# Optimization experiments

Hardware: AMD Instinct MI355X
Metric: run time of the kernel (lower is better)

## Reference

```python
import jax, jax.numpy as jnp
import numpy as np

HEADS, DH = 8, 32

def _ln(x):
    m = x.mean(-1, keepdims=True)
    v = ((x - m) ** 2).mean(-1, keepdims=True)
    return (x - m) * jax.lax.rsqrt(v + 1e-5)

def _attn(xq, xk, ei, ea, wq, wk, wv, we, wo):
    # one relation: q from dst-type nodes xq, k/v from src-type nodes xk
    Nd, Ns, E = xq.shape[0], xk.shape[0], ea.shape[0]
    src, dst = ei[0], ei[1]
    q = (xq @ wq).reshape(Nd, HEADS, DH)
    k = (xk @ wk).reshape(Ns, HEADS, DH)
    v = (xk @ wv).reshape(Ns, HEADS, DH)
    e = (ea @ we).reshape(E, HEADS, DH)
    s = jnp.sum(q[dst] * (k[src] + e), axis=-1) * (DH ** -0.5)  # (E, heads)
    m = jax.ops.segment_max(s, dst, num_segments=Nd)
    m = jnp.where(jnp.isfinite(m), m, 0.0)
    ex = jnp.exp(s - m[dst])
    den = jax.ops.segment_sum(ex, dst, num_segments=Nd)
    msg = jax.ops.segment_sum(ex[:, :, None] * (v[src] + e), dst, num_segments=Nd)
    msg = msg / (den[:, :, None] + 1e-9)
    return msg.reshape(Nd, HEADS * DH) @ wo

def setup_inputs() -> dict:
    key = jax.random.key(0)
    ks = list(jax.random.split(key, 24))
    N, H, ED, L, F = 18432, 256, 64, 2, 512
    EA, ES = 294912, 65536
    nrm = lambda k, shp, s=1.0: jax.random.normal(k, shp, dtype=jnp.float32) * s
    inp = {}
    inp['all_feats_left'] = nrm(ks[0], (N, H))
    inp['all_feats_right'] = nrm(ks[1], (N, H))
    inp['ea_ll'] = nrm(ks[2], (EA, ED))
    inp['ea_rr'] = nrm(ks[3], (EA, ED))
    inp['ea_lr'] = nrm(ks[4], (ES, ED))
    inp['ea_rl'] = nrm(ks[5], (ES, ED))
    inp['ei_ll'] = jax.random.randint(ks[6], (2, EA), 0, N, dtype=jnp.int32)
    inp['ei_rr'] = jax.random.randint(ks[7], (2, EA), 0, N, dtype=jnp.int32)
    inp['ei_lr'] = jax.random.randint(ks[8], (2, ES), 0, N, dtype=jnp.int32)
    inp['ei_rl'] = jax.random.randint(ks[9], (2, ES), 0, N, dtype=jnp.int32)
    # relation order: 0=ll, 1=rr, 2=lr (src left -> dst right), 3=rl
    inp['Wq'] = nrm(ks[10], (L, 4, H, H), H ** -0.5)
    inp['Wk'] = nrm(ks[11], (L, 4, H, H), H ** -0.5)
    inp['Wv'] = nrm(ks[12], (L, 4, H, H), H ** -0.5)
    inp['We'] = nrm(ks[13], (L, 4, ED, H), ED ** -0.5)
    inp['Wo'] = nrm(ks[14], (L, 4, H, H), H ** -0.5)
    inp['ffn_w1'] = nrm(ks[15], (L, 2, H, F), H ** -0.5)
    inp['ffn_b1'] = jnp.zeros((L, 2, F), jnp.float32)
    inp['ffn_w2'] = nrm(ks[16], (L, 2, F, H), F ** -0.5)
    inp['ffn_b2'] = jnp.zeros((L, 2, H), jnp.float32)
    inp['head_w1'] = nrm(ks[17], (H, H), H ** -0.5)
    inp['head_b1'] = jnp.zeros((H,), jnp.float32)
    inp['head_w2'] = nrm(ks[18], (H, 7), H ** -0.5)
    inp['head_b2'] = jnp.zeros((7,), jnp.float32)
    inp['action_start'] = 2048  # slice(K, None), K current nodes per arm
    return inp

def reference(all_feats_left, all_feats_right, ea_ll, ea_rr, ea_lr, ea_rl,
              Wq, Wk, Wv, We, Wo, ffn_w1, ffn_b1, ffn_w2, ffn_b2,
              head_w1, head_b1, head_w2, head_b2,
              ei_ll, ei_rr, ei_lr, ei_rl, action_start):
    xl, xr = all_feats_left, all_feats_right
    L = Wq.shape[0]
    for l in range(L):
        agg_l = (_attn(xl, xl, ei_ll, ea_ll, Wq[l, 0], Wk[l, 0], Wv[l, 0], We[l, 0], Wo[l, 0])
                 + _attn(xl, xr, ei_rl, ea_rl, Wq[l, 3], Wk[l, 3], Wv[l, 3], We[l, 3], Wo[l, 3]))
        agg_r = (_attn(xr, xr, ei_rr, ea_rr, Wq[l, 1], Wk[l, 1], Wv[l, 1], We[l, 1], Wo[l, 1])
                 + _attn(xr, xl, ei_lr, ea_lr, Wq[l, 2], Wk[l, 2], Wv[l, 2], We[l, 2], Wo[l, 2]))
        xl = _ln(xl + agg_l)
        xr = _ln(xr + agg_r)
        xl = _ln(xl + jax.nn.gelu(xl @ ffn_w1[l, 0] + ffn_b1[l, 0]) @ ffn_w2[l, 0] + ffn_b2[l, 0])
        xr = _ln(xr + jax.nn.gelu(xr @ ffn_w1[l, 1] + ffn_b1[l, 1]) @ ffn_w2[l, 1] + ffn_b2[l, 1])
    la = xl[action_start:]
    ra = xr[action_start:]
    head = lambda z: jax.nn.gelu(z @ head_w1 + head_b1) @ head_w2 + head_b2
    return head(la), head(ra)
```

## Files before the change

### kernel.cpp

```cpp
#include <hip/hip_runtime.h>
#include <math.h>

typedef __attribute__((ext_vector_type(8))) short short8;
typedef __attribute__((ext_vector_type(4))) float f32x4;

__device__ __forceinline__ unsigned short f2bf(float f) {
  unsigned u = __builtin_bit_cast(unsigned, f);
  u += 0x7fff + ((u >> 16) & 1);
  return (unsigned short)(u >> 16);
}
__device__ __forceinline__ float bf2f(unsigned short h) {
  unsigned u = ((unsigned)h) << 16;
  return __builtin_bit_cast(float, u);
}
__device__ __forceinline__ float gelu_f(float x) {
  const float c0 = 0.7978845608028654f;
  return 0.5f * x * (1.0f + tanhf(c0 * (x + 0.044715f * x * x * x)));
}
__device__ __forceinline__ void gload16(const unsigned short* g, unsigned short* l) {
  __builtin_amdgcn_global_load_lds(
      (const __attribute__((address_space(1))) unsigned int*)g,
      (__attribute__((address_space(3))) unsigned int*)l, 16, 0, 0);
}
__device__ __forceinline__ int ileave512(int cc) {
  const int base = (cc & 256) ? 4 : 0;
  const int c2 = cc & 255;
  return (c2 >> 2) * 8 + base + (c2 & 3);
}

__device__ __forceinline__ void kloop_db(
    const unsigned short* gA0, const unsigned short* gA1,
    const unsigned short* gB0, const unsigned short* gB1,
    unsigned short* As, unsigned short* Bs,
    int lo0, int lo1, const int* roffA, const int* roffB,
    f32x4 (&acc)[4][4], int K)
{
  gload16(gA0, As + lo0);
  gload16(gA1, As + lo1);
  gload16(gB0, Bs + lo0);
  gload16(gB1, Bs + lo1);
  int cur = 0;
  for (int k0 = 32; k0 < K; k0 += 32) {
    const int nb = (cur ^ 1) * 4096;
    gload16(gA0 + k0, As + nb + lo0);
    gload16(gA1 + k0, As + nb + lo1);
    gload16(gB0 + k0, Bs + nb + lo0);
    gload16(gB1 + k0, Bs + nb + lo1);
    __builtin_amdgcn_sched_barrier(0);
    asm volatile("s_waitcnt vmcnt(4)" ::: "memory");
    __builtin_amdgcn_s_barrier();
    __builtin_amdgcn_sched_barrier(0);
    const int cb = cur * 4096;
    short8 af[4], bfr[4];
#pragma unroll
    for (int m = 0; m < 4; ++m) af[m] = *(const short8*)(As + cb + roffA[m]);
#pragma unroll
    for (int n = 0; n < 4; ++n) bfr[n] = *(const short8*)(Bs + cb + roffB[n]);
#pragma unroll
    for (int m = 0; m < 4; ++m)
#pragma unroll
      for (int n = 0; n < 4; ++n)
        acc[m][n] = __builtin_amdgcn_mfma_f32_16x16x32_bf16(af[m], bfr[n], acc[m][n], 0, 0, 0);
    __builtin_amdgcn_sched_barrier(0);
    __builtin_amdgcn_s_barrier();
    cur ^= 1;
  }
  __builtin_amdgcn_sched_barrier(0);
  asm volatile("s_waitcnt vmcnt(0)" ::: "memory");
  __builtin_amdgcn_s_barrier();
  __builtin_amdgcn_sched_barrier(0);
  const int cb = cur * 4096;
  short8 af[4], bfr[4];
#pragma unroll
  for (int m = 0; m < 4; ++m) af[m] = *(const short8*)(As + cb + roffA[m]);
#pragma unroll
  for (int n = 0; n < 4; ++n) bfr[n] = *(const short8*)(Bs + cb + roffB[n]);
#pragma unroll
  for (int m = 0; m < 4; ++m)
#pragma unroll
    for (int n = 0; n < 4; ++n)
      acc[m][n] = __builtin_amdgcn_mfma_f32_16x16x32_bf16(af[m], bfr[n], acc[m][n], 0, 0, 0);
}

__global__ __launch_bounds__(256)
void gemm_qkv_k(const unsigned short* __restrict__ A0, const unsigned short* __restrict__ A1,
                const unsigned short* __restrict__ BT0, const unsigned short* __restrict__ BT1,
                unsigned short* __restrict__ qT0, unsigned short* __restrict__ qT1,
                unsigned short* __restrict__ kvS0, unsigned short* __restrict__ kvS1,
                unsigned short* __restrict__ kvX0, unsigned short* __restrict__ kvX1,
                int M)
{
  const int z = blockIdx.z;
  const unsigned short* A  = z ? A1  : A0;
  const unsigned short* BT = z ? BT1 : BT0;
  unsigned short* qT  = z ? qT1  : qT0;
  unsigned short* kvS = z ? kvS1 : kvS0;
  unsigned short* kvX = z ? kvX1 : kvX0;
  const int K = 256, lda = 256;

  __shared__ __align__(16) unsigned short As[2 * 4096];
  __shared__ __align__(16) unsigned short Bs[2 * 4096];
  const int tid = threadIdx.x;
  const int bm = blockIdx.x * 128, bn = blockIdx.y * 128;
  const int lane = tid & 63, w = tid >> 6;
  const int wr = w >> 1, wc = w & 1;
  const int l15 = lane & 15, kg = lane >> 4;
  const int srow0 = w * 16 + (lane >> 2);
  const int srow1 = 64 + srow0;
  const int sslot = lane & 3;
  const int koff0 = (((sslot - (srow0 >> 1)) & 3)) * 8;
  const int koff1 = (((sslot - (srow1 >> 1)) & 3)) * 8;
  const unsigned short* gA0 = A + (size_t)(bm + srow0) * lda + koff0;
  const unsigned short* gA1 = A + (size_t)(bm + srow1) * lda + koff1;
  const unsigned short* gB0 = BT + (size_t)(bn + srow0) * K + koff0;
  const unsigned short* gB1 = BT + (size_t)(bn + srow1) * K + koff1;
  const int lo0 = w * 512;
  const int lo1 = 2048 + w * 512;

  int roffA[4], roffB[4];
#pragma unroll
  for (int m = 0; m < 4; ++m) {
    int row = wr * 64 + m * 16 + l15;
    roffA[m] = row * 32 + ((kg + (row >> 1)) & 3) * 8;
  }
#pragma unroll
  for (int n = 0; n < 4; ++n) {
    int col = wc * 64 + n * 16 + l15;
    roffB[n] = col * 32 + ((kg + (col >> 1)) & 3) * 8;
  }

  f32x4 acc[4][4] = {};
  kloop_db(gA0, gA1, gB0, gB1, As, Bs, lo0, lo1, roffA, roffB, acc, K);

#pragma unroll
  for (int m = 0; m < 4; ++m) {
#pragma unroll
    for (int n = 0; n < 4; ++n) {
      int col = bn + wc * 64 + n * 16 + l15;
      f32x4 v = acc[m][n];
#pragma unroll
      for (int r2 = 0; r2 < 4; ++r2) {
        int row = bm + wr * 64 + m * 16 + kg * 4 + r2;
        unsigned short bv = f2bf(v[r2]);
        if (col < 768) {
          qT[(size_t)row * 1536 + col] = bv;
        } else if (col < 1280) {
          kvS[(size_t)row * 512 + ileave512(col - 768)] = bv;
        } else if (col < 2048) {
          qT[(size_t)row * 1536 + 768 + (col - 1280)] = bv;
        } else {
          kvX[(size_t)row * 512 + ileave512(col - 2048)] = bv;
        }
      }
    }
  }
}

template<bool BIAS, bool GELU>
__global__ __launch_bounds__(256)
void gemm_mfma2_k(const unsigned short* __restrict__ A0, const unsigned short* __restrict__ A1,
                  int lda,
                  const unsigned short* __restrict__ BT0, const unsigned short* __restrict__ BT1,
                  const float* __restrict__ bias0, const float* __restrict__ bias1,
                  float* __restrict__ Cf0, float* __restrict__ Cf1, int Sf, int ldf,
                  unsigned short* __restrict__ Cb10, unsigned short* __restrict__ Cb11,
                  int S2, int ldb1,
                  unsigned short* __restrict__ Cb20, unsigned short* __restrict__ Cb21, int ldb2,
                  int M, int N, int K)
{
  const int z = blockIdx.z;
  const unsigned short* A  = z ? A1  : A0;
  const unsigned short* BT = z ? BT1 : BT0;
  const float* bias        = z ? bias1 : bias0;
  float* Cf                = z ? Cf1 : Cf0;
  unsigned short* Cb1      = z ? Cb11 : Cb10;
  unsigned short* Cb2      = z ? Cb21 : Cb20;

  __shared__ __align__(16) unsigned short As[2 * 4096];
  __shared__ __align__(16) unsigned short Bs[2 * 4096];
  const int tid = threadIdx.x;
  const int bm = blockIdx.x * 128, bn = blockIdx.y * 128;
  const int lane = tid & 63, w = tid >> 6;
  const int wr = w >> 1, wc = w & 1;
  const int l15 = lane & 15, kg = lane >> 4;
  const int srow0 = w * 16 + (lane >> 2);
  const int srow1 = 64 + srow0;
  const int sslot = lane & 3;
  const int koff0 = (((sslot - (srow0 >> 1)) & 3)) * 8;
  const int koff1 = (((sslot - (srow1 >> 1)) & 3)) * 8;
  const unsigned short* gA0 = A + (size_t)(bm + srow0) * lda + koff0;
  const unsigned short* gA1 = A + (size_t)(bm + srow1) * lda + koff1;
  const unsigned short* gB0 = BT + (size_t)(bn + srow0) * K + koff0;
  const unsigned short* gB1 = BT + (size_t)(bn + srow1) * K + koff1;
  const int lo0 = w * 512;
  const int lo1 = 2048 + w * 512;

  int roffA[4], roffB[4];
#pragma unroll
  for (int m = 0; m < 4; ++m) {
    int row = wr * 64 + m * 16 + l15;
    roffA[m] = row * 32 + ((kg + (row >> 1)) & 3) * 8;
  }
#pragma unroll
  for (int n = 0; n < 4; ++n) {
    int col = wc * 64 + n * 16 + l15;
    roffB[n] = col * 32 + ((kg + (col >> 1)) & 3) * 8;
  }

  f32x4 acc[4][4] = {};
  kloop_db(gA0, gA1, gB0, gB1, As, Bs, lo0, lo1, roffA, roffB, acc, K);

#pragma unroll
  for (int m = 0; m < 4; ++m) {
#pragma unroll
    for (int n = 0; n < 4; ++n) {
      int col = bn + wc * 64 + n * 16 + l15;
      float bv = BIAS ? bias[col] : 0.f;
      f32x4 v = acc[m][n];
#pragma unroll
      for (int r2 = 0; r2 < 4; ++r2) {
        int row = bm + wr * 64 + m * 16 + kg * 4 + r2;
        float val = v[r2] + bv;
        if (GELU) val = gelu_f(val);
        if (col < Sf) {
          Cf[(size_t)row * ldf + col] = val;
        } else if (col < S2) {
          Cb1[(size_t)row * ldb1 + (col - Sf)] = f2bf(val);
        } else {
          Cb2[(size_t)row * ldb2 + (col - S2)] = f2bf(val);
        }
      }
    }
  }
}

template<bool BIAS>
__global__ __launch_bounds__(256)
void gemm_k2(const float* __restrict__ A0, const float* __restrict__ A1,
             const float* __restrict__ B, const float* __restrict__ bias,
             float* __restrict__ C0, float* __restrict__ C1,
             int M, int N, int K)
{
  const float* A = blockIdx.z ? A1 : A0;
  float* C = blockIdx.z ? C1 : C0;
  __shared__ float As[16][132];
  __shared__ float Bs[16][132];
  const int tid = threadIdx.x;
  const int tx = tid & 15, ty = tid >> 4;
  const int bm = blockIdx.x * 128;
  float acc[8][8];
#pragma unroll
  for (int i = 0; i < 8; ++i)
#pragma unroll
    for (int j = 0; j < 8; ++j) acc[i][j] = 0.f;
  const int ar = tid >> 1;
  const int ac = (tid & 1) * 8;
  const int br = tid >> 4;
  const int bc = (tid & 15) * 8;
  for (int k0 = 0; k0 < K; k0 += 16) {
    {
      float av[8] = {0,0,0,0,0,0,0,0};
      if (bm + ar < M) {
        const float* app = A + (size_t)(bm + ar) * K + (k0 + ac);
        float4 a0 = *(const float4*)app;
        float4 a1 = *(const float4*)(app + 4);
        av[0]=a0.x; av[1]=a0.y; av[2]=a0.z; av[3]=a0.w;
        av[4]=a1.x; av[5]=a1.y; av[6]=a1.z; av[7]=a1.w;
      }
#pragma unroll
      for (int i = 0; i < 8; ++i) As[ac + i][ar] = av[i];
    }
    {
      float bv[8] = {0,0,0,0,0,0,0,0};
      const float* bpp = B + (size_t)(k0 + br) * N + bc;
#pragma unroll
      for (int i = 0; i < 8; ++i) { if (bc + i < N) bv[i] = bpp[i]; }
#pragma unroll
      for (int i = 0; i < 8; ++i) Bs[br][bc + i] = bv[i];
    }
    __syncthreads();
#pragma unroll
    for (int kk = 0; kk < 16; ++kk) {
      float a[8], b[8];
      float4 t0 = *(const float4*)&As[kk][ty * 8];
      float4 t1 = *(const float4*)&As[kk][ty * 8 + 4];
      float4 u0 = *(const float4*)&Bs[kk][tx * 8];
      float4 u1 = *(const float4*)&Bs[kk][tx * 8 + 4];
      a[0]=t0.x;a[1]=t0.y;a[2]=t0.z;a[3]=t0.w;a[4]=t1.x;a[5]=t1.y;a[6]=t1.z;a[7]=t1.w;
      b[0]=u0.x;b[1]=u0.y;b[2]=u0.z;b[3]=u0.w;b[4]=u1.x;b[5]=u1.y;b[6]=u1.z;b[7]=u1.w;
#pragma unroll
      for (int i = 0; i < 8; ++i)
#pragma unroll
        for (int j = 0; j < 8; ++j)
          acc[i][j] = fmaf(a[i], b[j], acc[i][j]);
    }
    __syncthreads();
  }
#pragma unroll
  for (int i = 0; i < 8; ++i) {
    int row = bm + ty * 8 + i;
    if (row >= M) continue;
    int colg = tx * 8;
    float* cp = C + (size_t)row * N + colg;
#pragma unroll
    for (int j = 0; j < 8; ++j) {
      int cc = colg + j;
      if (cc < N) {
        float val = acc[i][j];
        if (BIAS) val += bias[cc];
        cp[j] = val;
      }
    }
  }
}

__global__ void tc_k(const float* __restrict__ in, unsigned short* __restrict__ out,
                     int K, int N, int inStride, int outStride, int rowOff, int totK, int kOff)
{
  const int mat = blockIdx.y;
  const int idx = blockIdx.x * 256 + threadIdx.x;
  if (idx >= N * K) return;
  const int n = idx / K, k = idx - n * K;
  out[(size_t)mat * outStride + (size_t)(rowOff + n) * totK + kOff + k] =
      f2bf(in[(size_t)mat * inStride + (size_t)k * N + n]);
}

__global__ void tc_all_k(const float* __restrict__ Wq, const float* __restrict__ Wk,
                         const float* __restrict__ Wv, unsigned short* __restrict__ BTall)
{
  const int part = blockIdx.z;
  const int slot = blockIdx.y;
  const int l = slot >> 1, zz = slot & 1;
  const int self = l * 4 + zz;
  const int crossq = l * 4 + (zz ? 2 : 3);
  const int crosskv = l * 4 + (zz ? 3 : 2);
  const float* in; int mat, rowOff;
  switch (part) {
    case 0: in = Wq; mat = self;    rowOff = 0;    break;
    case 1: in = Wk; mat = self;    rowOff = 768;  break;
    case 2: in = Wv; mat = self;    rowOff = 1024; break;
    case 3: in = Wq; mat = crossq;  rowOff = 1280; break;
    case 4: in = Wk; mat = crosskv; rowOff = 2048; break;
    default:in = Wv; mat = crosskv; rowOff = 2304; break;
  }
  const int idx = blockIdx.x * 256 + threadIdx.x;
  const int n = idx >> 8, k = idx & 255;
  BTall[(size_t)slot * 655360 + (size_t)(rowOff + n) * 256 + k] =
      f2bf(in[(size_t)mat * 65536 + (size_t)k * 256 + n]);
}

__global__ __launch_bounds__(256)
void wqe2_k(unsigned short* __restrict__ BTall, const float* __restrict__ We)
{
  const int which = blockIdx.z;
  const int slot = blockIdx.y;
  const int l = slot >> 1, zz = slot & 1;
  const int mat = which ? (l * 4 + (zz ? 2 : 3)) : (l * 4 + zz);
  const int baseQ = which ? 1280 : 0;
  const int baseT = which ? 1536 : 256;
  const int oc = blockIdx.x;
  const int g = oc >> 6, cc = oc & 63;
  const int kin = threadIdx.x;
  const float* wrow = We + (size_t)mat * 16384 + (size_t)cc * 256 + g * 32;
  const unsigned short* bq = BTall + (size_t)slot * 655360 + (size_t)(baseQ + g * 32) * 256 + kin;
  float acc = 0.f;
#pragma unroll 8
  for (int d = 0; d < 32; ++d)
    acc += bf2f(bq[(size_t)d * 256]) * wrow[d];
  BTall[(size_t)slot * 655360 + (size_t)(baseT + oc) * 256 + kin] = f2bf(acc);
}

__global__ void wo_tc_k(const float* __restrict__ Wo, unsigned short* __restrict__ BTwoF)
{
  const int mat = blockIdx.y;
  const int idx = blockIdx.x * 256 + threadIdx.x;
  const int n = idx >> 8, k = idx & 255;
  const int l = mat >> 2, i = mat & 3;
  const int side = (i == 1 || i == 2) ? 1 : 0;
  const int base = (i >= 2) ? 768 : 0;
  BTwoF[(size_t)(l * 2 + side) * 393216 + (size_t)n * 1536 + base + k] =
      f2bf(Wo[(size_t)mat * 65536 + (size_t)k * 256 + n]);
}

__global__ __launch_bounds__(256)
void wc_k(const float* __restrict__ We, const float* __restrict__ Wo,
          unsigned short* __restrict__ BTwoF)
{
  const int mat = blockIdx.y;
  const int j = blockIdx.x;
  const int h = j >> 6, c = j & 63;
  const int n = threadIdx.x;
  const float* wep = We + (size_t)mat * 16384 + (size_t)c * 256 + h * 32;
  const float* wop = Wo + (size_t)mat * 65536 + (size_t)(h * 32) * 256 + n;
  float acc = 0.f;
#pragma unroll 8
  for (int d = 0; d < 32; ++d)
    acc += wep[d] * wop[(size_t)d * 256];
  const int l = mat >> 2, i = mat & 3;
  const int side = (i == 1 || i == 2) ? 1 : 0;
  const int base = (i >= 2) ? 768 : 0;
  BTwoF[(size_t)(l * 2 + side) * 393216 + (size_t)n * 1536 + base + 256 + j] = f2bf(acc);
}

__global__ __launch_bounds__(256)
void edge4_k(const int* __restrict__ o0, const int* __restrict__ o1,
             const int* __restrict__ o2, const int* __restrict__ o3,
             const int2* __restrict__ p0, const int2* __restrict__ p1,
             const int2* __restrict__ p2, const int2* __restrict__ p3,
             const float* __restrict__ e0, const float* __restrict__ e1,
             const float* __restrict__ e2, const float* __restrict__ e3,
             unsigned short* q0, unsigned short* q1,
             unsigned short* q2, unsigned short* q3,
             const unsigned short* __restrict__ k0, const unsigned short* __restrict__ k1,
             const unsigned short* __restrict__ k2, const unsigned short* __restrict__ k3,
             int Nn)
{
  const int y = blockIdx.y;
  const int* offs = (y == 0) ? o0 : (y == 1) ? o1 : (y == 2) ? o2 : o3;
  const int2* pairs = (y == 0) ? p0 : (y == 1) ? p1 : (y == 2) ? p2 : p3;
  const float* ea = (y == 0) ? e0 : (y == 1) ? e1 : (y == 2) ? e2 : e3;
  unsigned short* qTmsg = (y == 0) ? q0 : (y == 1) ? q1 : (y == 2) ? q2 : q3;
  const unsigned short* kv = (y == 0) ? k0 : (y == 1) ? k1 : (y == 2) ? k2 : k3;
  const int wv = (blockIdx.x * blockDim.x + threadIdx.x) >> 6;
  if (wv >= Nn) return;
  const int lane = threadIdx.x & 63;
  const int g = lane >> 3, p = lane & 7;
  const float scale = 0.17677669529663687f;
  const ushort4 qu = *(const ushort4*)(qTmsg + (size_t)wv * 1536 + lane * 4);
  const float qx = bf2f(qu.x), qy = bf2f(qu.y), qz = bf2f(qu.z), qw = bf2f(qu.w);
  const unsigned short* Tp = qTmsg + (size_t)wv * 1536 + 256 + g * 64 + p * 8;
  const ushort4 tu0 = *(const ushort4*)Tp;
  const ushort4 tu1 = *(const ushort4*)(Tp + 4);
  const float Ta0 = bf2f(tu0.x), Ta1 = bf2f(tu0.y), Ta2 = bf2f(tu0.z), Ta3 = bf2f(tu0.w);
  const float Tc0 = bf2f(tu1.x), Tc1 = bf2f(tu1.y), Tc2 = bf2f(tu1.z), Tc3 = bf2f(tu1.w);
  float m = -INFINITY, den = 0.f;
  float ax = 0.f, ay = 0.f, az = 0.f, aw = 0.f;
  float G[8] = {0,0,0,0,0,0,0,0};
  const int e0i = __builtin_amdgcn_readfirstlane(offs[wv]);
  const int e1i = __builtin_amdgcn_readfirstlane(offs[wv + 1]);
  for (int j = e0i; j < e1i; j += 2) {
    const bool hasB = (j + 1) < e1i;
    const int2 prA = pairs[j];
    const int2 prB = hasB ? pairs[j + 1] : prA;
    const f32x4* epA = (const f32x4*)(ea + (size_t)prA.x * 64 + p * 8);
    const f32x4* epB = (const f32x4*)(ea + (size_t)prB.x * 64 + p * 8);
    const f32x4 a0 = __builtin_nontemporal_load(epA);
    const f32x4 a1 = __builtin_nontemporal_load(epA + 1);
    const f32x4 b0 = __builtin_nontemporal_load(epB);
    const f32x4 b1 = __builtin_nontemporal_load(epB + 1);
    const short8 kvA = *(const short8*)(kv + (size_t)prA.y * 512 + lane * 8);
    const short8 kvB = *(const short8*)(kv + (size_t)prB.y * 512 + lane * 8);
    float pA = qx * bf2f((unsigned short)kvA[0]) + qy * bf2f((unsigned short)kvA[1])
             + qz * bf2f((unsigned short)kvA[2]) + qw * bf2f((unsigned short)kvA[3]);
    pA += a0[0]*Ta0 + a0[1]*Ta1 + a0[2]*Ta2 + a0[3]*Ta3;
    pA += a1[0]*Tc0 + a1[1]*Tc1 + a1[2]*Tc2 + a1[3]*Tc3;
    float pB = qx * bf2f((unsigned short)kvB[0]) + qy * bf2f((unsigned short)kvB[1])
             + qz * bf2f((unsigned short)kvB[2]) + qw * bf2f((unsigned short)kvB[3]);
    pB += b0[0]*Ta0 + b0[1]*Ta1 + b0[2]*Ta2 + b0[3]*Ta3;
    pB += b1[0]*Tc0 + b1[1]*Tc1 + b1[2]*Tc2 + b1[3]*Tc3;
    pA += __shfl_xor(pA, 1, 64); pA += __shfl_xor(pA, 2, 64); pA += __shfl_xor(pA, 4, 64);
    pB += __shfl_xor(pB, 1, 64); pB += __shfl_xor(pB, 2, 64); pB += __shfl_xor(pB, 4, 64);
    const float sA = pA * scale;
    const float sB = hasB ? pB * scale : -INFINITY;
    const float mn = fmaxf(m, fmaxf(sA, sB));
    const float corr = __expf(m - mn);
    const float wA = __expf(sA - mn);
    const float wB = __expf(sB - mn);
    m = mn;
    den = den * corr + wA + wB;
    ax = ax * corr + wA * bf2f((unsigned short)kvA[4]) + wB * bf2f((unsigned short)kvB[4]);
    ay = ay * corr + wA * bf2f((unsigned short)kvA[5]) + wB * bf2f((unsigned short)kvB[5]);
    az = az * corr + wA * bf2f((unsigned short)kvA[6]) + wB * bf2f((unsigned short)kvB[6]);
    aw = aw * corr + wA * bf2f((unsigned short)kvA[7]) + wB * bf2f((unsigned short)kvB[7]);
    G[0] = G[0] * corr + wA * a0[0] + wB * b0[0];
    G[1] = G[1] * corr + wA * a0[1] + wB * b0[1];
    G[2] = G[2] * corr + wA * a0[2] + wB * b0[2];
    G[3] = G[3] * corr + wA * a0[3] + wB * b0[3];
    G[4] = G[4] * corr + wA * a1[0] + wB * b1[0];
    G[5] = G[5] * corr + wA * a1[1] + wB * b1[1];
    G[6] = G[6] * corr + wA * a1[2] + wB * b1[2];
    G[7] = G[7] * corr + wA * a1[3] + wB * b1[3];
  }
  const float inv = 1.f / (den + 1e-9f);
  ushort4 o;
  o.x = f2bf(ax * inv); o.y = f2bf(ay * inv);
  o.z = f2bf(az * inv); o.w = f2bf(aw * inv);
  *(ushort4*)(qTmsg + (size_t)wv * 1536 + lane * 4) = o;
  short8 gn;
#pragma unroll
  for (int i = 0; i < 8; ++i) gn[i] = (short)f2bf(G[i] * inv);
  *(short8*)(qTmsg + (size_t)wv * 1536 + 256 + g * 64 + p * 8) = gn;
}

__global__ __launch_bounds__(256)
void add_ln2_k(unsigned short* __restrict__ xbL, const unsigned short* __restrict__ addL,
               unsigned short* __restrict__ xbR, const unsigned short* __restrict__ addR, int Nn)
{
  unsigned short* xb = blockIdx.y ? xbR : xbL;
  const unsigned short* add = blockIdx.y ? addR : addL;
  const int wv = (blockIdx.x * blockDim.x + threadIdx.x) >> 6;
  if (wv >= Nn) return;
  const int lane = threadIdx.x & 63;
  ushort4 xu = *(const ushort4*)(xb + (size_t)wv * 256 + lane * 4);
  ushort4 au = *(const ushort4*)(add + (size_t)wv * 256 + lane * 4);
  float4 y;
  y.x = bf2f(xu.x) + bf2f(au.x); y.y = bf2f(xu.y) + bf2f(au.y);
  y.z = bf2f(xu.z) + bf2f(au.z); y.w = bf2f(xu.w) + bf2f(au.w);
  float s = y.x + y.y + y.z + y.w;
#pragma unroll
  for (int msk = 1; msk < 64; msk <<= 1) s += __shfl_xor(s, msk, 64);
  const float mean = s * (1.f / 256.f);
  float4 d;
  d.x = y.x - mean; d.y = y.y - mean; d.z = y.z - mean; d.w = y.w - mean;
  float sq = d.x*d.x + d.y*d.y + d.z*d.z + d.w*d.w;
#pragma unroll
  for (int msk = 1; msk < 64; msk <<= 1) sq += __shfl_xor(sq, msk, 64);
  const float r = rsqrtf(sq * (1.f / 256.f) + 1e-5f);
  ushort4 ob;
  ob.x = f2bf(d.x * r); ob.y = f2bf(d.y * r);
  ob.z = f2bf(d.z * r); ob.w = f2bf(d.w * r);
  *(ushort4*)(xb + (size_t)wv * 256 + lane * 4) = ob;
}

__global__ void cvt_x2_k(const float* __restrict__ aL, unsigned short* __restrict__ xbL,
                         const float* __restrict__ aR, unsigned short* __restrict__ xbR, int n4)
{
  const float* a = blockIdx.y ? aR : aL;
  unsigned short* xb = blockIdx.y ? xbR : xbL;
  int i = blockIdx.x * 256 + threadIdx.x;
  if (i >= n4) return;
  float4 v = ((const float4*)a)[i];
  ushort4 b;
  b.x = f2bf(v.x); b.y = f2bf(v.y); b.z = f2bf(v.z); b.w = f2bf(v.w);
  ((ushort4*)xb)[i] = b;
}

__global__ void zero4_k(int* p, int n) {
  int i = blockIdx.x * 256 + threadIdx.x;
  if (i < n) p[i] = 0;
}
__global__ void hist4_k(const int* d0, const int* d1, const int* d2, const int* d3,
                        int E0, int E1, int E2, int E3, int* cnt, int Nn) {
  const int s = blockIdx.y;
  const int* d = (s == 0) ? d0 : (s == 1) ? d1 : (s == 2) ? d2 : d3;
  const int E = (s == 0) ? E0 : (s == 1) ? E1 : (s == 2) ? E2 : E3;
  int e = blockIdx.x * 256 + threadIdx.x;
  if (e < E) atomicAdd(&cnt[s * Nn + d[e]], 1);
}
__global__ __launch_bounds__(256)
void scan4_k(const int* __restrict__ cnt, int* __restrict__ offs, int* __restrict__ cursor, int Nn)
{
  __shared__ int sums[256];
  const int s = blockIdx.x;
  const int t = threadIdx.x;
  const int* c = cnt + (size_t)s * Nn;
  int* o = offs + (size_t)s * (Nn + 1);
  int* cur = cursor + (size_t)s * Nn;
  const int chunk = (Nn + 255) / 256;
  const int base = t * chunk;
  int sl = 0;
  for (int i = 0; i < chunk; ++i) {
    int idx = base + i;
    if (idx < Nn) sl += c[idx];
  }
  sums[t] = sl;
  __syncthreads();
  for (int off = 1; off < 256; off <<= 1) {
    int val = (t >= off) ? sums[t - off] : 0;
    __syncthreads();
    sums[t] += val;
    __syncthreads();
  }
  int run = (t == 0) ? 0 : sums[t - 1];
  for (int i = 0; i < chunk; ++i) {
    int idx = base + i;
    if (idx < Nn) { o[idx] = run; cur[idx] = run; run += c[idx]; }
  }
  if (t == 255) o[Nn] = run;
}
__global__ void scatter4_k(const int* e0p, const int* e1p, const int* e2p, const int* e3p,
                           int E0, int E1, int E2, int E3, int* cursor,
                           int2* p0, int2* p1, int2* p2, int2* p3, int Nn) {
  const int s = blockIdx.y;
  const int* ei = (s == 0) ? e0p : (s == 1) ? e1p : (s == 2) ? e2p : e3p;
  int2* po = (s == 0) ? p0 : (s == 1) ? p1 : (s == 2) ? p2 : p3;
  const int E = (s == 0) ? E0 : (s == 1) ? E1 : (s == 2) ? E2 : E3;
  int e = blockIdx.x * 256 + threadIdx.x;
  if (e < E) {
    int pos = atomicAdd(&cursor[s * Nn + ei[E + e]], 1);
    po[pos] = make_int2(e, ei[e]);
  }
}

extern "C" void kernel_launch(void* const* d_in, const int* in_sizes, int n_in,
                              void* d_out, int out_size, void* d_ws, size_t ws_size,
                              hipStream_t stream)
{
  (void)n_in; (void)ws_size;
  const float* afl = (const float*)d_in[0];
  const float* afr = (const float*)d_in[1];
  const float* eaA[4] = {(const float*)d_in[2], (const float*)d_in[3],
                         (const float*)d_in[4], (const float*)d_in[5]};
  const int* eiA[4] = {(const int*)d_in[6], (const int*)d_in[7],
                       (const int*)d_in[8], (const int*)d_in[9]};
  const float* Wq  = (const float*)d_in[10];
  const float* Wk  = (const float*)d_in[11];
  const float* Wv  = (const float*)d_in[12];
  const float* We  = (const float*)d_in[13];
  const float* Wo  = (const float*)d_in[14];
  const float* fw1 = (const float*)d_in[15];
  const float* fb1 = (const float*)d_in[16];
  const float* fw2 = (const float*)d_in[17];
  const float* fb2 = (const float*)d_in[18];
  const float* hw1 = (const float*)d_in[19];
  const float* hb1 = (const float*)d_in[20];
  const float* hw2 = (const float*)d_in[21];
  const float* hb2 = (const float*)d_in[22];

  const int Nn = in_sizes[0] / 256;
  const int E[4] = {in_sizes[2] / 64, in_sizes[3] / 64, in_sizes[4] / 64, in_sizes[5] / 64};
  const int Mh = out_size / 14;
  const int astart = Nn - Mh;
  float* out = (float*)d_out;

  char* wsp = (char*)d_ws;
  auto alloc = [&](size_t bytes) -> void* {
    void* pp = (void*)wsp;
    wsp += (bytes + 255) & ~(size_t)255;
    return pp;
  };
  unsigned short* xlb = (unsigned short*)alloc((size_t)Nn * 256 * 2);
  unsigned short* xrb = (unsigned short*)alloc((size_t)Nn * 256 * 2);
  unsigned short* aggLb = (unsigned short*)alloc((size_t)Nn * 256 * 2);
  unsigned short* aggRb = (unsigned short*)alloc((size_t)Nn * 256 * 2);
  unsigned short* qTmsgA = (unsigned short*)alloc((size_t)Nn * 1536 * 2);
  unsigned short* qTmsgB = (unsigned short*)alloc((size_t)Nn * 1536 * 2);
  unsigned short* kvSA = (unsigned short*)alloc((size_t)Nn * 512 * 2);
  unsigned short* kvSB = (unsigned short*)alloc((size_t)Nn * 512 * 2);
  unsigned short* kvXL = (unsigned short*)alloc((size_t)Nn * 512 * 2);
  unsigned short* kvXR = (unsigned short*)alloc((size_t)Nn * 512 * 2);
  unsigned short* BTall = (unsigned short*)alloc((size_t)4 * 655360 * 2);
  unsigned short* BTwoF = (unsigned short*)alloc((size_t)4 * 256 * 1536 * 2);
  unsigned short* BTf1  = (unsigned short*)alloc((size_t)4 * 512 * 256 * 2);
  unsigned short* BTf2  = (unsigned short*)alloc((size_t)4 * 256 * 512 * 2);
  unsigned short* BTh1  = (unsigned short*)alloc((size_t)256 * 256 * 2);
  int* offs4 = (int*)alloc((size_t)4 * (Nn + 1) * 4);
  int* cnt4  = (int*)alloc((size_t)4 * Nn * 4);
  int* cur4  = (int*)alloc((size_t)4 * Nn * 4);
  int2* pairs[4];
  for (int s = 0; s < 4; ++s) pairs[s] = (int2*)alloc((size_t)E[s] * 8);

  const dim3 B256(256);
  const int wgNodes = (Nn * 64 + 255) / 256;
  int maxE = E[0];
  for (int s = 1; s < 4; ++s) if (E[s] > maxE) maxE = E[s];

  cvt_x2_k<<<dim3((Nn * 64 + 255) / 256, 2), B256, 0, stream>>>(afl, xlb, afr, xrb, Nn * 64);
  zero4_k<<<dim3((4 * Nn + 255) / 256), B256, 0, stream>>>(cnt4, 4 * Nn);
  {
    dim3 gh((maxE + 255) / 256, 4);
    hist4_k<<<gh, B256, 0, stream>>>(eiA[0] + E[0], eiA[1] + E[1], eiA[2] + E[2], eiA[3] + E[3],
                                     E[0], E[1], E[2], E[3], cnt4, Nn);
    scan4_k<<<dim3(4), B256, 0, stream>>>(cnt4, offs4, cur4, Nn);
    scatter4_k<<<gh, B256, 0, stream>>>(eiA[0], eiA[1], eiA[2], eiA[3],
                                        E[0], E[1], E[2], E[3], cur4,
                                        pairs[0], pairs[1], pairs[2], pairs[3], Nn);
  }
  {
    tc_all_k<<<dim3(256, 4, 6), B256, 0, stream>>>(Wq, Wk, Wv, BTall);
    wqe2_k<<<dim3(512, 4, 2), B256, 0, stream>>>(BTall, We);
    wo_tc_k<<<dim3(256, 8), B256, 0, stream>>>(Wo, BTwoF);
    wc_k<<<dim3(512, 8), B256, 0, stream>>>(We, Wo, BTwoF);
    tc_k<<<dim3((131072 + 255) / 256, 4), B256, 0, stream>>>(fw1, BTf1, 256, 512, 131072, 131072, 0, 256, 0);
    tc_k<<<dim3((131072 + 255) / 256, 4), B256, 0, stream>>>(fw2, BTf2, 512, 256, 131072, 131072, 0, 512, 0);
    tc_k<<<dim3((65536 + 255) / 256, 1), B256, 0, stream>>>(hw1, BTh1, 256, 256, 0, 0, 0, 256, 0);
  }

  auto mfma2 = [&](const unsigned short* A0, const unsigned short* A1, int lda,
                   const unsigned short* BT0, const unsigned short* BT1,
                   const float* bias0, const float* bias1,
                   float* Cf0, float* Cf1, int Sf, int ldf,
                   unsigned short* Cb10, unsigned short* Cb11, int S2, int ldb1,
                   unsigned short* Cb20, unsigned short* Cb21, int ldb2,
                   int M, int N, int K, bool biasf, bool gelu) {
    dim3 g(M / 128, N / 128, 2);
    if (biasf && gelu)
      gemm_mfma2_k<true, true ><<<g, B256, 0, stream>>>(A0, A1, lda, BT0, BT1, bias0, bias1,
          Cf0, Cf1, Sf, ldf, Cb10, Cb11, S2, ldb1, Cb20, Cb21, ldb2, M, N, K);
    else if (biasf)
      gemm_mfma2_k<true, false><<<g, B256, 0, stream>>>(A0, A1, lda, BT0, BT1, bias0, bias1,
          Cf0, Cf1, Sf, ldf, Cb10, Cb11, S2, ldb1, Cb20, Cb21, ldb2, M, N, K);
    else
      gemm_mfma2_k<false, false><<<g, B256, 0, stream>>>(A0, A1, lda, BT0, BT1, bias0, bias1,
          Cf0, Cf1, Sf, ldf, Cb10, Cb11, S2, ldb1, Cb20, Cb21, ldb2, M, N, K);
  };

  for (int l = 0; l < 2; ++l) {
    gemm_qkv_k<<<dim3(Nn / 128, 20, 2), B256, 0, stream>>>(
        xlb, xrb,
        BTall + (size_t)(l * 2 + 0) * 655360, BTall + (size_t)(l * 2 + 1) * 655360,
        qTmsgA, qTmsgB, kvSA, kvSB, kvXL, kvXR, Nn);
    edge4_k<<<dim3(wgNodes, 4), B256, 0, stream>>>(
        offs4, offs4 + (size_t)(Nn + 1), offs4 + (size_t)3 * (Nn + 1), offs4 + (size_t)2 * (Nn + 1),
        pairs[0], pairs[1], pairs[3], pairs[2],
        eaA[0], eaA[1], eaA[3], eaA[2],
        qTmsgA, qTmsgB, qTmsgA + 768, qTmsgB + 768,
        kvSA, kvSB, kvXR, kvXL, Nn);
    mfma2(qTmsgA, qTmsgB, 1536, BTwoF + (size_t)(l*2+0)*393216, BTwoF + (size_t)(l*2+1)*393216,
          nullptr, nullptr, nullptr, nullptr, 0, 0, aggLb, aggRb, 256, 256,
          nullptr, nullptr, 0, Nn, 256, 1536, false, false);
    add_ln2_k<<<dim3(wgNodes, 2), B256, 0, stream>>>(xlb, aggLb, xrb, aggRb, Nn);
    const int fL = l * 2 + 0, fR = l * 2 + 1;
    mfma2(xlb, xrb, 256, BTf1 + (size_t)fL*131072, BTf1 + (size_t)fR*131072,
          fb1 + (size_t)fL*512, fb1 + (size_t)fR*512, nullptr, nullptr, 0, 0,
          kvSA, kvSB, 512, 512, nullptr, nullptr, 0, Nn, 512, 256, true, true);
    mfma2(kvSA, kvSB, 512, BTf2 + (size_t)fL*131072, BTf2 + (size_t)fR*131072,
          fb2 + (size_t)fL*256, fb2 + (size_t)fR*256, nullptr, nullptr, 0, 0,
          aggLb, aggRb, 256, 256, nullptr, nullptr, 0, Nn, 256, 512, true, false);
    add_ln2_k<<<dim3(wgNodes, 2), B256, 0, stream>>>(xlb, aggLb, xrb, aggRb, Nn);
  }
  float* h1L = (float*)kvSA;
  float* h1R = (float*)kvSB;
  mfma2(xlb + (size_t)astart * 256, xrb + (size_t)astart * 256, 256, BTh1, BTh1,
        hb1, hb1, h1L, h1R, 256, 256, nullptr, nullptr, 0, 0, nullptr, nullptr, 0,
        Mh, 256, 256, true, true);
  gemm_k2<true><<<dim3(Mh / 128, 1, 2), B256, 0, stream>>>(h1L, h1R, hw2, hb2,
                                                           out, out + (size_t)Mh * 7, Mh, 7, 256);
}
```

Baseline: 1.029 ms.

## Fuse output-projection and FFN2 GEMMs with residual add and LayerNorm

Adds a GEMM kernel whose block covers 64 full rows of 256 columns, so the epilogue can add the residual, reduce the row mean and variance across waves through shared memory, and write the normalized bf16 result in place. It replaces the separate Wo GEMM, FFN2 GEMM and add_ln2 kernels, removing the bf16 agg intermediate round trips and two launches per layer. The cost is a narrower grid (Nn/64 blocks per arm) with a single wave column per block, one-pass variance (E[x²]−mean²), and residual loads that are not coalesced.

```diff
diff --git a/kernel.cpp b/kernel.cpp
--- a/kernel.cpp
+++ b/kernel.cpp
@@ -80,6 +80,149 @@
 #pragma unroll
     for (int n = 0; n < 4; ++n)
       acc[m][n] = __builtin_amdgcn_mfma_f32_16x16x32_bf16(af[m], bfr[n], acc[m][n], 0, 0, 0);
+}
+
+template<bool BIAS>
+__global__ __launch_bounds__(256)
+void gemm_ln_k(const unsigned short* __restrict__ A0, const unsigned short* __restrict__ A1,
+               int lda,
+               const unsigned short* __restrict__ BT0, const unsigned short* __restrict__ BT1,
+               const float* __restrict__ bias0, const float* __restrict__ bias1,
+               unsigned short* __restrict__ xb0, unsigned short* __restrict__ xb1,
+               int K)
+{
+  const int z = blockIdx.z;
+  const unsigned short* A  = z ? A1 : A0;
+  const unsigned short* BT = z ? BT1 : BT0;
+  const float* bias        = z ? bias1 : bias0;
+  unsigned short* xb       = z ? xb1 : xb0;
+
+  __shared__ __align__(16) unsigned short As[2 * 2048];
+  __shared__ __align__(16) unsigned short Bs[2 * 8192];
+  __shared__ float redS[64][4];
+  __shared__ float redQ[64][4];
+
+  const int tid = threadIdx.x;
+  const int bm = blockIdx.x * 64;
+  const int lane = tid & 63, w = tid >> 6;
+  const int l15 = lane & 15, kg = lane >> 4;
+  const int sslot = lane & 3;
+  const int srowA = w * 16 + (lane >> 2);
+  const int koffA = ((sslot - (srowA >> 1)) & 3) * 8;
+  const unsigned short* gA = A + (size_t)(bm + srowA) * lda + koffA;
+  const int loA = w * 512;
+  const unsigned short* gB[4];
+  int loB[4];
+#pragma unroll
+  for (int h = 0; h < 4; ++h) {
+    int srowB = h * 64 + w * 16 + (lane >> 2);
+    int koffB = ((sslot - (srowB >> 1)) & 3) * 8;
+    gB[h] = BT + (size_t)srowB * K + koffB;
+    loB[h] = h * 2048 + w * 512;
+  }
+  int roffA[4], roffB[4];
+#pragma unroll
+  for (int m = 0; m < 4; ++m) {
+    int row = m * 16 + l15;
+    roffA[m] = row * 32 + ((kg + (row >> 1)) & 3) * 8;
+  }
+#pragma unroll
+  for (int n = 0; n < 4; ++n) {
+    int col = w * 64 + n * 16 + l15;
+    roffB[n] = col * 32 + ((kg + (col >> 1)) & 3) * 8;
+  }
+
+  f32x4 acc[4][4] = {};
+  gload16(gA, As + loA);
+#pragma unroll
+  for (int h = 0; h < 4; ++h) gload16(gB[h], Bs + loB[h]);
+  int cur = 0;
+  for (int k0 = 32; k0 < K; k0 += 32) {
+    const int nbA = (cur ^ 1) * 2048, nbB = (cur ^ 1) * 8192;
+    gload16(gA + k0, As + nbA + loA);
+#pragma unroll
+    for (int h = 0; h < 4; ++h) gload16(gB[h] + k0, Bs + nbB + loB[h]);
+    __builtin_amdgcn_sched_barrier(0);
+    asm volatile("s_waitcnt vmcnt(5)" ::: "memory");
+    __builtin_amdgcn_s_barrier();
+    __builtin_amdgcn_sched_barrier(0);
+    const int cbA = cur * 2048, cbB = cur * 8192;
+    short8 af[4], bfr[4];
+#pragma unroll
+    for (int m = 0; m < 4; ++m) af[m] = *(const short8*)(As + cbA + roffA[m]);
+#pragma unroll
+    for (int n = 0; n < 4; ++n) bfr[n] = *(const short8*)(Bs + cbB + roffB[n]);
+#pragma unroll
+    for (int m = 0; m < 4; ++m)
+#pragma unroll
+      for (int n = 0; n < 4; ++n)
+        acc[m][n] = __builtin_amdgcn_mfma_f32_16x16x32_bf16(af[m], bfr[n], acc[m][n], 0, 0, 0);
+    __builtin_amdgcn_sched_barrier(0);
+    __builtin_amdgcn_s_barrier();
+    cur ^= 1;
+  }
+  __builtin_amdgcn_sched_barrier(0);
+  asm volatile("s_waitcnt vmcnt(0)" ::: "memory");
+  __builtin_amdgcn_s_barrier();
+  __builtin_amdgcn_sched_barrier(0);
+  {
+    const int cbA = cur * 2048, cbB = cur * 8192;
+    short8 af[4], bfr[4];
+#pragma unroll
+    for (int m = 0; m < 4; ++m) af[m] = *(const short8*)(As + cbA + roffA[m]);
+#pragma unroll
+    for (int n = 0; n < 4; ++n) bfr[n] = *(const short8*)(Bs + cbB + roffB[n]);
+#pragma unroll
+    for (int m = 0; m < 4; ++m)
+#pragma unroll
+      for (int n = 0; n < 4; ++n)
+        acc[m][n] = __builtin_amdgcn_mfma_f32_16x16x32_bf16(af[m], bfr[n], acc[m][n], 0, 0, 0);
+  }
+
+  float bv[4];
+#pragma unroll
+  for (int n = 0; n < 4; ++n) bv[n] = BIAS ? bias[w * 64 + n * 16 + l15] : 0.f;
+
+#pragma unroll
+  for (int m = 0; m < 4; ++m) {
+#pragma unroll
+    for (int r2 = 0; r2 < 4; ++r2) {
+      const int row = m * 16 + kg * 4 + r2;
+      float rs = 0.f, rq = 0.f;
+#pragma unroll
+      for (int n = 0; n < 4; ++n) {
+        const int col = w * 64 + n * 16 + l15;
+        float val = acc[m][n][r2] + bv[n]
+                  + bf2f(xb[(size_t)(bm + row) * 256 + col]);
+        acc[m][n][r2] = val;
+        rs += val;
+        rq += val * val;
+      }
+      rs += __shfl_xor(rs, 1, 64); rq += __shfl_xor(rq, 1, 64);
+      rs += __shfl_xor(rs, 2, 64); rq += __shfl_xor(rq, 2, 64);
+      rs += __shfl_xor(rs, 4, 64); rq += __shfl_xor(rq, 4, 64);
+      rs += __shfl_xor(rs, 8, 64); rq += __shfl_xor(rq, 8, 64);
+      if (l15 == 0) { redS[row][w] = rs; redQ[row][w] = rq; }
+    }
+  }
+  __syncthreads();
+#pragma unroll
+  for (int m = 0; m < 4; ++m) {
+#pragma unroll
+    for (int r2 = 0; r2 < 4; ++r2) {
+      const int row = m * 16 + kg * 4 + r2;
+      const float s = redS[row][0] + redS[row][1] + redS[row][2] + redS[row][3];
+      const float q = redQ[row][0] + redQ[row][1] + redQ[row][2] + redQ[row][3];
+      const float mean = s * (1.f / 256.f);
+      const float var = q * (1.f / 256.f) - mean * mean;
+      const float r = rsqrtf(var + 1e-5f);
+#pragma unroll
+      for (int n = 0; n < 4; ++n) {
+        const int col = w * 64 + n * 16 + l15;
+        xb[(size_t)(bm + row) * 256 + col] = f2bf((acc[m][n][r2] - mean) * r);
+      }
+    }
+  }
 }
 
 __global__ __launch_bounds__(256)
@@ -215,12 +358,12 @@
 #pragma unroll
     for (int n = 0; n < 4; ++n) {
       int col = bn + wc * 64 + n * 16 + l15;
-      float bv = BIAS ? bias[col] : 0.f;
+      float bvv = BIAS ? bias[col] : 0.f;
       f32x4 v = acc[m][n];
 #pragma unroll
       for (int r2 = 0; r2 < 4; ++r2) {
         int row = bm + wr * 64 + m * 16 + kg * 4 + r2;
-        float val = v[r2] + bv;
+        float val = v[r2] + bvv;
         if (GELU) val = gelu_f(val);
         if (col < Sf) {
           Cf[(size_t)row * ldf + col] = val;
@@ -271,12 +414,12 @@
       for (int i = 0; i < 8; ++i) As[ac + i][ar] = av[i];
     }
     {
-      float bv[8] = {0,0,0,0,0,0,0,0};
+      float bvv[8] = {0,0,0,0,0,0,0,0};
       const float* bpp = B + (size_t)(k0 + br) * N + bc;
 #pragma unroll
-      for (int i = 0; i < 8; ++i) { if (bc + i < N) bv[i] = bpp[i]; }
-#pragma unroll
-      for (int i = 0; i < 8; ++i) Bs[br][bc + i] = bv[i];
+      for (int i = 0; i < 8; ++i) { if (bc + i < N) bvv[i] = bpp[i]; }
+#pragma unroll
+      for (int i = 0; i < 8; ++i) Bs[br][bc + i] = bvv[i];
     }
     __syncthreads();
 #pragma unroll
@@ -492,36 +635,6 @@
   *(short8*)(qTmsg + (size_t)wv * 1536 + 256 + g * 64 + p * 8) = gn;
 }
 
-__global__ __launch_bounds__(256)
-void add_ln2_k(unsigned short* __restrict__ xbL, const unsigned short* __restrict__ addL,
-               unsigned short* __restrict__ xbR, const unsigned short* __restrict__ addR, int Nn)
-{
-  unsigned short* xb = blockIdx.y ? xbR : xbL;
-  const unsigned short* add = blockIdx.y ? addR : addL;
-  const int wv = (blockIdx.x * blockDim.x + threadIdx.x) >> 6;
-  if (wv >= Nn) return;
-  const int lane = threadIdx.x & 63;
-  ushort4 xu = *(const ushort4*)(xb + (size_t)wv * 256 + lane * 4);
-  ushort4 au = *(const ushort4*)(add + (size_t)wv * 256 + lane * 4);
-  float4 y;
-  y.x = bf2f(xu.x) + bf2f(au.x); y.y = bf2f(xu.y) + bf2f(au.y);
-  y.z = bf2f(xu.z) + bf2f(au.z); y.w = bf2f(xu.w) + bf2f(au.w);
-  float s = y.x + y.y + y.z + y.w;
-#pragma unroll
-  for (int msk = 1; msk < 64; msk <<= 1) s += __shfl_xor(s, msk, 64);
-  const float mean = s * (1.f / 256.f);
-  float4 d;
-  d.x = y.x - mean; d.y = y.y - mean; d.z = y.z - mean; d.w = y.w - mean;
-  float sq = d.x*d.x + d.y*d.y + d.z*d.z + d.w*d.w;
-#pragma unroll
-  for (int msk = 1; msk < 64; msk <<= 1) sq += __shfl_xor(sq, msk, 64);
-  const float r = rsqrtf(sq * (1.f / 256.f) + 1e-5f);
-  ushort4 ob;
-  ob.x = f2bf(d.x * r); ob.y = f2bf(d.y * r);
-  ob.z = f2bf(d.z * r); ob.w = f2bf(d.w * r);
-  *(ushort4*)(xb + (size_t)wv * 256 + lane * 4) = ob;
-}
-
 __global__ void cvt_x2_k(const float* __restrict__ aL, unsigned short* __restrict__ xbL,
                          const float* __restrict__ aR, unsigned short* __restrict__ xbR, int n4)
 {
@@ -631,8 +744,6 @@
   };
   unsigned short* xlb = (unsigned short*)alloc((size_t)Nn * 256 * 2);
   unsigned short* xrb = (unsigned short*)alloc((size_t)Nn * 256 * 2);
-  unsigned short* aggLb = (unsigned short*)alloc((size_t)Nn * 256 * 2);
-  unsigned short* aggRb = (unsigned short*)alloc((size_t)Nn * 256 * 2);
   unsigned short* qTmsgA = (unsigned short*)alloc((size_t)Nn * 1536 * 2);
   unsigned short* qTmsgB = (unsigned short*)alloc((size_t)Nn * 1536 * 2);
   unsigned short* kvSA = (unsigned short*)alloc((size_t)Nn * 512 * 2);
@@ -644,6 +755,8 @@
   unsigned short* BTf1  = (unsigned short*)alloc((size_t)4 * 512 * 256 * 2);
   unsigned short* BTf2  = (unsigned short*)alloc((size_t)4 * 256 * 512 * 2);
   unsigned short* BTh1  = (unsigned short*)alloc((size_t)256 * 256 * 2);
+  float* h1L = (float*)alloc((size_t)Mh * 256 * 4);
+  float* h1R = (float*)alloc((size_t)Mh * 256 * 4);
   int* offs4 = (int*)alloc((size_t)4 * (Nn + 1) * 4);
   int* cnt4  = (int*)alloc((size_t)4 * Nn * 4);
   int* cur4  = (int*)alloc((size_t)4 * Nn * 4);
@@ -706,21 +819,19 @@
         eaA[0], eaA[1], eaA[3], eaA[2],
         qTmsgA, qTmsgB, qTmsgA + 768, qTmsgB + 768,
         kvSA, kvSB, kvXR, kvXL, Nn);
-    mfma2(qTmsgA, qTmsgB, 1536, BTwoF + (size_t)(l*2+0)*393216, BTwoF + (size_t)(l*2+1)*393216,
-          nullptr, nullptr, nullptr, nullptr, 0, 0, aggLb, aggRb, 256, 256,
-          nullptr, nullptr, 0, Nn, 256, 1536, false, false);
-    add_ln2_k<<<dim3(wgNodes, 2), B256, 0, stream>>>(xlb, aggLb, xrb, aggRb, Nn);
+    gemm_ln_k<false><<<dim3(Nn / 64, 1, 2), B256, 0, stream>>>(
+        qTmsgA, qTmsgB, 1536,
+        BTwoF + (size_t)(l*2+0)*393216, BTwoF + (size_t)(l*2+1)*393216,
+        nullptr, nullptr, xlb, xrb, 1536);
     const int fL = l * 2 + 0, fR = l * 2 + 1;
     mfma2(xlb, xrb, 256, BTf1 + (size_t)fL*131072, BTf1 + (size_t)fR*131072,
           fb1 + (size_t)fL*512, fb1 + (size_t)fR*512, nullptr, nullptr, 0, 0,
           kvSA, kvSB, 512, 512, nullptr, nullptr, 0, Nn, 512, 256, true, true);
-    mfma2(kvSA, kvSB, 512, BTf2 + (size_t)fL*131072, BTf2 + (size_t)fR*131072,
-          fb2 + (size_t)fL*256, fb2 + (size_t)fR*256, nullptr, nullptr, 0, 0,
-          aggLb, aggRb, 256, 256, nullptr, nullptr, 0, Nn, 256, 512, true, false);
-    add_ln2_k<<<dim3(wgNodes, 2), B256, 0, stream>>>(xlb, aggLb, xrb, aggRb, Nn);
-  }
-  float* h1L = (float*)kvSA;
-  float* h1R = (float*)kvSB;
+    gemm_ln_k<true><<<dim3(Nn / 64, 1, 2), B256, 0, stream>>>(
+        kvSA, kvSB, 512,
+        BTf2 + (size_t)fL*131072, BTf2 + (size_t)fR*131072,
+        fb2 + (size_t)fL*256, fb2 + (size_t)fR*256, xlb, xrb, 512);
+  }
   mfma2(xlb + (size_t)astart * 256, xrb + (size_t)astart * 256, 256, BTh1, BTh1,
         hb1, hb1, h1L, h1R, 256, 256, nullptr, nullptr, 0, 0, nullptr, nullptr, 0,
         Mh, 256, 256, true, true);
```

Measured after the change: 1.107 ms. 7.6% more time.
